# Performance work log

Hardware: AMD Instinct MI355X
Metric: run time of the kernel (lower is better)

## Reference

```python
import jax, jax.numpy as jnp
import numpy as np
import math

B, T, D, La, Lr = 8, 128, 512, 2, 2
H = La + Lr
DK = D // H  # 128
DFF = 4 * D


def _gelu(x):
    # BERT tanh-approx GELU, matching the torch module exactly
    return 0.5 * x * (1.0 + jnp.tanh(math.sqrt(2.0 / math.pi) * (x + 0.044715 * x ** 3)))


def _ln(x, g, b, eps=1e-5):
    mu = jnp.mean(x, axis=-1, keepdims=True)
    var = jnp.mean((x - mu) ** 2, axis=-1, keepdims=True)
    return (x - mu) * jax.lax.rsqrt(var + eps) * g + b


def setup_inputs() -> dict:
    key = jax.random.key(0)
    ks = jax.random.split(key, 16)
    n = lambda k, s, sc=1.0: jax.random.normal(k, s, dtype=jnp.float32) * sc
    return {
        'x': n(ks[0], (B, T, D)),
        'mask': jnp.ones((B, 1, T, T), dtype=jnp.int32),
        'abs_kernel': n(ks[1], (La, B, T, D)),
        'rel_kernel': n(ks[2], (Lr, B, T, T, D)),
        'Wc': n(ks[3], (3, D, D), 0.02), 'bc': jnp.zeros((3, D), jnp.float32),
        'Wpq': n(ks[4], (La, D, DK), 0.02), 'bpq': jnp.zeros((La, DK), jnp.float32),
        'Wpk': n(ks[5], (La, D, DK), 0.02), 'bpk': jnp.zeros((La, DK), jnp.float32),
        'Wrk': n(ks[6], (Lr, D, DK), 0.02), 'brk': jnp.zeros((Lr, DK), jnp.float32),
        'rel_bias': n(ks[7], (Lr, DK), 0.02),
        'Wo': n(ks[8], (D, D), 0.02), 'bo': jnp.zeros((D,), jnp.float32),
        'W1': n(ks[9], (D, DFF), 0.02), 'b1': jnp.zeros((DFF,), jnp.float32),
        'W2': n(ks[10], (DFF, D), 0.02), 'b2': jnp.zeros((D,), jnp.float32),
        'ln1_g': jnp.ones((D,), jnp.float32), 'ln1_b': jnp.zeros((D,), jnp.float32),
        'ln2_g': jnp.ones((D,), jnp.float32), 'ln2_b': jnp.zeros((D,), jnp.float32),
    }


def _attention(h, mask, abs_kernel, rel_kernel, Wc, bc, Wpq, bpq, Wpk, bpk,
               Wrk, brk, rel_bias, Wo, bo):
    b, t = h.shape[0], h.shape[1]
    # content projections: [3,B,T,D] -> [3,B,H,T,DK]
    qkv = jnp.einsum('btd,cde->cbte', h, Wc) + bc[:, None, None, :]
    qkv = qkv.reshape(3, b, t, H, DK).transpose(0, 1, 3, 2, 4)
    q, k, v = qkv[0], qkv[1], qkv[2]
    # absolute-position heads
    Pq = jnp.einsum('abtd,ade->bate', abs_kernel, Wpq) + bpq[None, :, None, :]
    Pk = jnp.einsum('abtd,ade->bate', abs_kernel, Wpk) + bpk[None, :, None, :]
    abs_scores = jnp.einsum('blid,bljd->blij', q[:, :La] + Pq, k[:, :La] + Pk)
    # relative-position heads (R: [B,Lr,T,T,DK])
    R = jnp.einsum('abijd,ade->baije', rel_kernel, Wrk) + brk[None, :, None, None, :]
    Xq = q[:, La:]
    rel_scores = jnp.einsum('blid,bljd->blij', Xq, k[:, La:])
    rel_scores = rel_scores + jnp.einsum('blid,blijd->blij', Xq + rel_bias[None, :, None, :], R)
    scores = jnp.concatenate([abs_scores, rel_scores], axis=1) * (DK ** -0.5)
    scores = jnp.where(mask == 0, jnp.float32(-1e9), scores)
    p_attn = jax.nn.softmax(scores, axis=-1)
    out = jnp.einsum('bhij,bhjd->bhid', p_attn, v)
    out = out.transpose(0, 2, 1, 3).reshape(b, t, H * DK)
    return out @ Wo + bo


def reference(x, mask, abs_kernel, rel_kernel, Wc, bc, Wpq, bpq, Wpk, bpk,
              Wrk, brk, rel_bias, Wo, bo, W1, b1, W2, b2,
              ln1_g, ln1_b, ln2_g, ln2_b):
    # pre-LN sublayer 1: attention
    h = _ln(x, ln1_g, ln1_b)
    x = x + _attention(h, mask, abs_kernel, rel_kernel, Wc, bc, Wpq, bpq,
                       Wpk, bpk, Wrk, brk, rel_bias, Wo, bo)
    # pre-LN sublayer 2: FFN with tanh-GELU
    h2 = _ln(x, ln2_g, ln2_b)
    x = x + (_gelu(h2 @ W1 + b1) @ W2 + b2)
    return x
```

## Files before the change

kernel.cpp:

```cpp
#include <hip/hip_runtime.h>
#include <math.h>

static constexpr int Dc  = 512;
static constexpr int DKc = 128;

typedef __attribute__((ext_vector_type(8))) short short8v;
typedef __attribute__((ext_vector_type(4))) float f32x4;

static __device__ __forceinline__ ushort f2bf(float x) {
  unsigned u = __builtin_bit_cast(unsigned, x);
  unsigned r = (u + 0x7fffu + ((u >> 16) & 1u)) >> 16;
  return (ushort)r;
}

__device__ __forceinline__ float gelu_f(float v) {
  float t = tanhf(0.7978845608028654f * (v + 0.044715f * v * v * v));
  return 0.5f * v * (1.0f + t);
}

__global__ __launch_bounds__(256) void ln_kernel(const float* __restrict__ x,
    const float* __restrict__ g, const float* __restrict__ bb,
    ushort* __restrict__ out)
{
  int gid = blockIdx.x * 256 + threadIdx.x;
  int row = gid >> 6;
  int lane = threadIdx.x & 63;
  const float* xr = x + (size_t)row * Dc + lane * 8;
  float4 a = *(const float4*)xr;
  float4 c = *(const float4*)(xr + 4);
  float s  = a.x + a.y + a.z + a.w + c.x + c.y + c.z + c.w;
  float ss = a.x*a.x + a.y*a.y + a.z*a.z + a.w*a.w
           + c.x*c.x + c.y*c.y + c.z*c.z + c.w*c.w;
  #pragma unroll
  for (int off = 32; off > 0; off >>= 1) {
    s  += __shfl_xor(s, off);
    ss += __shfl_xor(ss, off);
  }
  float mu  = s * (1.0f/512.0f);
  float var = ss * (1.0f/512.0f) - mu*mu;
  float rstd = rsqrtf(var + 1e-5f);
  const float* gp = g + lane*8;
  const float* bp = bb + lane*8;
  float4 g0 = *(const float4*)gp, g1 = *(const float4*)(gp+4);
  float4 b0 = *(const float4*)bp, b1 = *(const float4*)(bp+4);
  union { ushort u[8]; uint4 v; } pk;
  pk.u[0] = f2bf((a.x-mu)*rstd*g0.x + b0.x);
  pk.u[1] = f2bf((a.y-mu)*rstd*g0.y + b0.y);
  pk.u[2] = f2bf((a.z-mu)*rstd*g0.z + b0.z);
  pk.u[3] = f2bf((a.w-mu)*rstd*g0.w + b0.w);
  pk.u[4] = f2bf((c.x-mu)*rstd*g1.x + b1.x);
  pk.u[5] = f2bf((c.y-mu)*rstd*g1.y + b1.y);
  pk.u[6] = f2bf((c.z-mu)*rstd*g1.z + b1.z);
  pk.u[7] = f2bf((c.w-mu)*rstd*g1.w + b1.w);
  *(uint4*)(out + (size_t)row * Dc + lane * 8) = pk.v;
}

struct CvtTasks {
  const float* src[16];
  void* dst[16];
  int rows[16], cols[16], mode[16], aux[16], end[16];
  int n;
};

__global__ __launch_bounds__(256) void cvt_kernel(CvtTasks T)
{
  __shared__ ushort tile[64][65];
  int b = blockIdx.x, t = threadIdx.x;
  int ti = 0;
  while (b >= T.end[ti]) ++ti;
  int lb = b - (ti ? T.end[ti-1] : 0);
  const float* src = T.src[ti];
  int mode = T.mode[ti];
  if (mode == 0) {
    int R = T.rows[ti], C = T.cols[ti];
    int tpr = C >> 6;
    int tyy = lb / tpr, txx = lb - tyy * tpr;
    int r0 = tyy << 6, c0 = txx << 6;
    int lr = t >> 4, lc4 = (t & 15) << 2;
    #pragma unroll
    for (int i = 0; i < 4; ++i) {
      int row = i*16 + lr;
      float4 vv = *(const float4*)(src + (size_t)(r0+row)*C + c0 + lc4);
      tile[row][lc4+0] = f2bf(vv.x);
      tile[row][lc4+1] = f2bf(vv.y);
      tile[row][lc4+2] = f2bf(vv.z);
      tile[row][lc4+3] = f2bf(vv.w);
    }
    __syncthreads();
    ushort* dst = (ushort*)T.dst[ti];
    #pragma unroll
    for (int i = 0; i < 4; ++i) {
      int n = i*16 + lr;
      ushort4 o;
      o.x = tile[lc4+0][n];
      o.y = tile[lc4+1][n];
      o.z = tile[lc4+2][n];
      o.w = tile[lc4+3][n];
      *(ushort4*)(dst + (size_t)(c0+n)*R + r0 + lc4) = o;
    }
  } else if (mode == 1) {
    int idx = lb*2048 + t*8;
    float4 v0 = *(const float4*)(src + idx);
    float4 v1 = *(const float4*)(src + idx + 4);
    union { ushort u[8]; uint4 q; } pk;
    pk.u[0]=f2bf(v0.x); pk.u[1]=f2bf(v0.y); pk.u[2]=f2bf(v0.z); pk.u[3]=f2bf(v0.w);
    pk.u[4]=f2bf(v1.x); pk.u[5]=f2bf(v1.y); pk.u[6]=f2bf(v1.z); pk.u[7]=f2bf(v1.w);
    *(uint4*)((ushort*)T.dst[ti] + idx) = pk.q;
  } else {
    if (t < T.cols[ti]) {
      float* d = (float*)T.dst[ti];
      for (int r = 0; r < T.rows[ti]; ++r)
        d[(size_t)(2*r + T.aux[ti]) * T.cols[ti] + t] = src[(size_t)r * T.cols[ti] + t];
    }
  }
}

template<bool OUT_BF16, bool GELU_>
__device__ __forceinline__ void gemm64_body(
    const ushort* __restrict__ A, int lda,
    const ushort* __restrict__ Bt, int ldb,
    const float* __restrict__ bias,
    void* __restrict__ Cout, int ldc,
    int ksteps, int bm, int bn)
{
  __shared__ __align__(16) char smem[16384];
  char* asB = smem;
  char* bsB = smem + 8192;
  int tid = threadIdx.x;
  int lane = tid & 63, wid = tid >> 6;
  int wr = wid >> 1, wc = wid & 1;
  int l15 = lane & 15, kg = lane >> 4;
  f32x4 acc[2][2] = {};
  const ushort* Ab = A + (size_t)bm * lda;
  const ushort* Bb = Bt + (size_t)bn * ldb;
  int r0 = tid >> 3;
  int c16 = tid & 7;
  int wb0 = r0*128 + ((c16*16) ^ ((r0 & 7) << 4));
  int wb1 = (r0+32)*128 + ((c16*16) ^ ((r0 & 7) << 4));
  for (int ks = 0; ks < ksteps; ++ks) {
    int k0 = ks * 64;
    uint4 ra0 = *(const uint4*)(Ab + (size_t)r0*lda + k0 + c16*8);
    uint4 ra1 = *(const uint4*)(Ab + (size_t)(r0+32)*lda + k0 + c16*8);
    uint4 rb0 = *(const uint4*)(Bb + (size_t)r0*ldb + k0 + c16*8);
    uint4 rb1 = *(const uint4*)(Bb + (size_t)(r0+32)*ldb + k0 + c16*8);
    __syncthreads();
    *(uint4*)(asB + wb0) = ra0;  *(uint4*)(asB + wb1) = ra1;
    *(uint4*)(bsB + wb0) = rb0;  *(uint4*)(bsB + wb1) = rb1;
    __syncthreads();
    #pragma unroll
    for (int half = 0; half < 2; ++half) {
      int cb = half*64 + kg*16;
      short8v av[2], bv[2];
      #pragma unroll
      for (int m = 0; m < 2; ++m) {
        int r = wr*32 + m*16 + l15;
        av[m] = *(const short8v*)(asB + r*128 + (cb ^ ((r & 7) << 4)));
      }
      #pragma unroll
      for (int n = 0; n < 2; ++n) {
        int r = wc*32 + n*16 + l15;
        bv[n] = *(const short8v*)(bsB + r*128 + (cb ^ ((r & 7) << 4)));
      }
      #pragma unroll
      for (int m = 0; m < 2; ++m)
        #pragma unroll
        for (int n = 0; n < 2; ++n)
          acc[m][n] = __builtin_amdgcn_mfma_f32_16x16x32_bf16(av[m], bv[n], acc[m][n], 0, 0, 0);
    }
  }
  int orow0 = bm + wr*32 + kg*4;
  int ocol0 = bn + wc*32 + l15;
  #pragma unroll
  for (int m = 0; m < 2; ++m) {
    #pragma unroll
    for (int r = 0; r < 4; ++r) {
      int row = orow0 + m*16 + r;
      #pragma unroll
      for (int n = 0; n < 2; ++n) {
        int col = ocol0 + n*16;
        float val = acc[m][n][r];
        if (bias) val += bias[col];
        if (GELU_) val = gelu_f(val);
        if (OUT_BF16) ((ushort*)Cout)[(size_t)row*ldc + col] = f2bf(val);
        else          ((float*)Cout)[(size_t)row*ldc + col]  = val;
      }
    }
  }
}

template<bool OUT_BF16, bool GELU_>
__global__ __launch_bounds__(256) void g64(
    const ushort* __restrict__ A, int lda, long Abatch,
    const ushort* __restrict__ Bt, int ldb, long Bbatch,
    const float* __restrict__ bias, int biasStride,
    void* __restrict__ C, int ldc, long Cbatch,
    int ksteps)
{
  int z = blockIdx.z;
  const float* bz = bias ? bias + (size_t)z * biasStride : nullptr;
  void* Cz = OUT_BF16 ? (void*)((ushort*)C + (size_t)z*Cbatch)
                      : (void*)((float*)C + (size_t)z*Cbatch);
  gemm64_body<OUT_BF16, GELU_>(A + (size_t)z*Abatch, lda,
      Bt + (size_t)z*Bbatch, ldb, bz, Cz, ldc, ksteps,
      blockIdx.y*64, blockIdx.x*64);
}

__global__ __launch_bounds__(256) void qkvp_gemm(
    const ushort* __restrict__ h, const ushort* __restrict__ WcT,
    const float* __restrict__ bc, float* __restrict__ qkv,
    const ushort* __restrict__ absb, const ushort* __restrict__ Wp,
    const float* __restrict__ bqk, float* __restrict__ Pqk)
{
  int z = blockIdx.z;
  const ushort *A, *Bt;
  const float* bias;
  float* C;
  int ldc;
  if (z < 3) {
    A = h; Bt = WcT + (size_t)z*262144; bias = bc + z*512;
    C = qkv + (size_t)z*524288; ldc = 512;
  } else {
    if (blockIdx.x >= 2) return;
    int t = z - 3;
    A = absb + (size_t)(t >> 1)*524288;
    Bt = Wp + (size_t)t*65536;
    bias = bqk + t*128;
    C = Pqk + (size_t)t*131072; ldc = 128;
  }
  gemm64_body<false,false>(A, 512, Bt, 512, bias, C, ldc, 8,
      blockIdx.y*64, blockIdx.x*64);
}

__global__ __launch_bounds__(256) void fused_small(
    const float* __restrict__ q, const float* __restrict__ k,
    float* __restrict__ Pqk, const float* __restrict__ rel_bias,
    const float* __restrict__ brk, ushort* __restrict__ uinb,
    float* __restrict__ cvec)
{
  int tid = threadIdx.x;
  if (blockIdx.x < 1024) {
    int idx = blockIdx.x*256 + tid;
    int dk = idx & 127;
    int rest = idx >> 7;
    int m = rest & 1023;
    int a = rest >> 10;
    Pqk[idx + a*131072]     += q[(size_t)m*512 + a*128 + dk];
    Pqk[idx + (a+1)*131072] += k[(size_t)m*512 + a*128 + dk];
  } else {
    int blkk = blockIdx.x - 1024;
    int half = tid >> 7, t = tid & 127;
    int row = blkk*2 + half;
    int l = row >> 10, m = row & 1023;
    float val = q[(size_t)m*512 + (2+l)*128 + t] + rel_bias[l*128 + t];
    uinb[(size_t)row*128 + t] = f2bf(val);
    float p = brk[l*128 + t] * val;
    #pragma unroll
    for (int off = 32; off > 0; off >>= 1) p += __shfl_xor(p, off);
    __shared__ float red[4];
    if ((tid & 63) == 0) red[tid >> 6] = p;
    __syncthreads();
    if (tid == 0)   cvec[row] = red[0] + red[1];
    if (tid == 128) cvec[row] = red[2] + red[3];
  }
}

__global__ __launch_bounds__(256) void relattn_kernel(
    const float* __restrict__ rk, const float* __restrict__ u,
    const float* __restrict__ q, const float* __restrict__ k,
    const float* __restrict__ v, const float* __restrict__ cvec,
    const int* __restrict__ mask, ushort* __restrict__ attnob)
{
  int blk = blockIdx.x;
  int tid = threadIdx.x;
  int i = blk & 127, b = (blk >> 7) & 7, l = blk >> 10, h = 2 + l;
  int m_i = b*128 + i;
  __shared__ float qs[128], sc[128], ps[128], red[64], pvs[2][128], stat[2];
  int wave = tid >> 6, lane = tid & 63;
  const float* ur = u + ((size_t)l*1024 + m_i)*512 + lane*8;
  float4 uu0 = *(const float4*)ur;
  float4 uu1 = *(const float4*)(ur + 4);
  if (tid < 128) qs[tid] = q[(size_t)m_i*512 + h*128 + tid];
  __syncthreads();
  float xq0 = qs[lane*2], xq1 = qs[lane*2+1];
  const float* base = rk + (size_t)blk*65536 + lane*8;
  const float* kb = k + (size_t)(b*128)*512 + h*128 + lane*2;
  #pragma unroll 2
  for (int jj = 0; jj < 32; ++jj) {
    int j = wave*32 + jj;
    const float* r = base + (size_t)j*512;
    float4 r0 = *(const float4*)r;
    float4 r1 = *(const float4*)(r + 4);
    float2 kk = *(const float2*)(kb + (size_t)j*512);
    float s = r0.x*uu0.x + r0.y*uu0.y + r0.z*uu0.z + r0.w*uu0.w
            + r1.x*uu1.x + r1.y*uu1.y + r1.z*uu1.z + r1.w*uu1.w
            + kk.x*xq0 + kk.y*xq1;
    #pragma unroll
    for (int off = 32; off > 0; off >>= 1) s += __shfl_xor(s, off);
    if (lane == 0) sc[j] = s;
  }
  __syncthreads();
  if (tid < 128) {
    float sv = (sc[tid] + cvec[l*1024 + m_i]) * 0.088388347648318447f;
    if (mask[((size_t)(b*128) + i)*128 + tid] == 0) sv = -1e9f;
    sc[tid] = sv;
  }
  __syncthreads();
  if (tid < 64) red[tid] = fmaxf(sc[tid], sc[tid+64]);
  __syncthreads();
  if (tid < 64) {
    float m = red[tid];
    #pragma unroll
    for (int off = 32; off > 0; off >>= 1) m = fmaxf(m, __shfl_xor(m, off));
    if (tid == 0) stat[0] = m;
  }
  __syncthreads();
  if (tid < 128) ps[tid] = __expf(sc[tid] - stat[0]);
  __syncthreads();
  if (tid < 64) red[tid] = ps[tid] + ps[tid+64];
  __syncthreads();
  if (tid < 64) {
    float s = red[tid];
    #pragma unroll
    for (int off = 32; off > 0; off >>= 1) s += __shfl_xor(s, off);
    if (tid == 0) stat[1] = 1.0f / s;
  }
  __syncthreads();
  int hf = tid >> 7, dk = tid & 127;
  const float* vp = v + (size_t)(b*128 + hf*64)*512 + h*128 + dk;
  float o = 0.0f;
  #pragma unroll 4
  for (int jj = 0; jj < 64; ++jj) o += ps[hf*64 + jj] * vp[(size_t)jj*512];
  pvs[hf][dk] = o;
  __syncthreads();
  if (tid < 128)
    attnob[(size_t)m_i*512 + h*128 + tid] = f2bf((pvs[0][tid] + pvs[1][tid]) * stat[1]);
}

__global__ __launch_bounds__(128) void absattn_kernel(
    const float* __restrict__ Pqk, const float* __restrict__ v,
    const int* __restrict__ mask, ushort* __restrict__ attnob)
{
  int blk = blockIdx.x;
  int tid = threadIdx.x;
  int i = blk & 127;
  int bh = blk >> 7;
  int h = bh & 1;
  int b = bh >> 1;
  __shared__ float qsh[128], psh[128], redh[128];
  int m_i = b*128 + i;
  qsh[tid] = Pqk[(size_t)(2*h)*131072 + (size_t)m_i*128 + tid];
  __syncthreads();
  int j = tid, m_j = b*128 + j;
  const float* krow = Pqk + (size_t)(2*h+1)*131072 + (size_t)m_j*128;
  float dot = 0.0f;
  #pragma unroll
  for (int d = 0; d < 128; d += 4) {
    float4 kv = *(const float4*)(krow + d);
    dot += kv.x*qsh[d] + kv.y*qsh[d+1] + kv.z*qsh[d+2] + kv.w*qsh[d+3];
  }
  float s = dot * 0.088388347648318447f;
  if (mask[((size_t)(b*128) + i)*128 + j] == 0) s = -1e9f;
  redh[tid] = s;
  __syncthreads();
  #pragma unroll
  for (int off = 64; off > 0; off >>= 1) {
    if (tid < off) redh[tid] = fmaxf(redh[tid], redh[tid + off]);
    __syncthreads();
  }
  float mx = redh[0];
  __syncthreads();
  float e = __expf(s - mx);
  psh[tid] = e;
  redh[tid] = e;
  __syncthreads();
  #pragma unroll
  for (int off = 64; off > 0; off >>= 1) {
    if (tid < off) redh[tid] += redh[tid + off];
    __syncthreads();
  }
  float inv = 1.0f / redh[0];
  int dk = tid;
  const float* vp = v + (size_t)b*65536 + h*128 + dk;
  float o = 0.0f;
  for (int jj = 0; jj < 128; ++jj) o += psh[jj] * vp[(size_t)jj*512];
  attnob[(size_t)m_i*512 + h*128 + dk] = f2bf(o * inv);
}

__global__ __launch_bounds__(256) void reduce_ln_kernel(
    const float* __restrict__ wpart, const float* __restrict__ bo,
    const float* __restrict__ x, const float* __restrict__ g,
    const float* __restrict__ bb, float* __restrict__ x1,
    ushort* __restrict__ h2)
{
  int gid = blockIdx.x*256 + threadIdx.x;
  int row = gid >> 6, lane = threadIdx.x & 63;
  size_t off = (size_t)row*512 + lane*8;
  float4 a = *(const float4*)(x + off);
  float4 c = *(const float4*)(x + off + 4);
  #pragma unroll
  for (int sk = 0; sk < 4; ++sk) {
    float4 p0 = *(const float4*)(wpart + (size_t)sk*524288 + off);
    float4 p1 = *(const float4*)(wpart + (size_t)sk*524288 + off + 4);
    a.x += p0.x; a.y += p0.y; a.z += p0.z; a.w += p0.w;
    c.x += p1.x; c.y += p1.y; c.z += p1.z; c.w += p1.w;
  }
  float4 bo0 = *(const float4*)(bo + lane*8);
  float4 bo1 = *(const float4*)(bo + lane*8 + 4);
  a.x += bo0.x; a.y += bo0.y; a.z += bo0.z; a.w += bo0.w;
  c.x += bo1.x; c.y += bo1.y; c.z += bo1.z; c.w += bo1.w;
  *(float4*)(x1 + off) = a;
  *(float4*)(x1 + off + 4) = c;
  float s  = a.x + a.y + a.z + a.w + c.x + c.y + c.z + c.w;
  float ss = a.x*a.x + a.y*a.y + a.z*a.z + a.w*a.w
           + c.x*c.x + c.y*c.y + c.z*c.z + c.w*c.w;
  #pragma unroll
  for (int off2 = 32; off2 > 0; off2 >>= 1) {
    s  += __shfl_xor(s, off2);
    ss += __shfl_xor(ss, off2);
  }
  float mu  = s * (1.0f/512.0f);
  float var = ss * (1.0f/512.0f) - mu*mu;
  float rstd = rsqrtf(var + 1e-5f);
  float4 g0 = *(const float4*)(g + lane*8), g1 = *(const float4*)(g + lane*8 + 4);
  float4 b0 = *(const float4*)(bb + lane*8), b1 = *(const float4*)(bb + lane*8 + 4);
  union { ushort u[8]; uint4 v; } pk;
  pk.u[0] = f2bf((a.x-mu)*rstd*g0.x + b0.x);
  pk.u[1] = f2bf((a.y-mu)*rstd*g0.y + b0.y);
  pk.u[2] = f2bf((a.z-mu)*rstd*g0.z + b0.z);
  pk.u[3] = f2bf((a.w-mu)*rstd*g0.w + b0.w);
  pk.u[4] = f2bf((c.x-mu)*rstd*g1.x + b1.x);
  pk.u[5] = f2bf((c.y-mu)*rstd*g1.y + b1.y);
  pk.u[6] = f2bf((c.z-mu)*rstd*g1.z + b1.z);
  pk.u[7] = f2bf((c.w-mu)*rstd*g1.w + b1.w);
  *(uint4*)(h2 + off) = pk.v;
}

__global__ __launch_bounds__(256) void reduce_out_kernel(
    const float* __restrict__ fpart, const float* __restrict__ b2,
    const float* __restrict__ x1, float* __restrict__ out)
{
  int idx = blockIdx.x*256 + threadIdx.x;
  size_t o4 = (size_t)idx*4;
  float4 s = *(const float4*)(x1 + o4);
  #pragma unroll
  for (int sk = 0; sk < 4; ++sk) {
    float4 p = *(const float4*)(fpart + (size_t)sk*524288 + o4);
    s.x += p.x; s.y += p.y; s.z += p.z; s.w += p.w;
  }
  float4 bv = *(const float4*)(b2 + ((idx & 127)*4));
  s.x += bv.x; s.y += bv.y; s.z += bv.z; s.w += bv.w;
  *(float4*)(out + o4) = s;
}

extern "C" void kernel_launch(void* const* d_in, const int* in_sizes, int n_in,
                              void* d_out, int out_size, void* d_ws, size_t ws_size,
                              hipStream_t stream)
{
  const float* x         = (const float*)d_in[0];
  const int*   mask      = (const int*)  d_in[1];
  const float* abs_kernel= (const float*)d_in[2];
  const float* rel_kernel= (const float*)d_in[3];
  const float* Wc        = (const float*)d_in[4];
  const float* bc        = (const float*)d_in[5];
  const float* Wpq       = (const float*)d_in[6];
  const float* bpq       = (const float*)d_in[7];
  const float* Wpk       = (const float*)d_in[8];
  const float* bpk       = (const float*)d_in[9];
  const float* Wrk       = (const float*)d_in[10];
  const float* brk       = (const float*)d_in[11];
  const float* rel_bias  = (const float*)d_in[12];
  const float* Wo        = (const float*)d_in[13];
  const float* bo        = (const float*)d_in[14];
  const float* W1        = (const float*)d_in[15];
  const float* b1        = (const float*)d_in[16];
  const float* W2        = (const float*)d_in[17];
  const float* b2        = (const float*)d_in[18];
  const float* ln1g      = (const float*)d_in[19];
  const float* ln1b      = (const float*)d_in[20];
  const float* ln2g      = (const float*)d_in[21];
  const float* ln2b      = (const float*)d_in[22];

  float* ws = (float*)d_ws;
  float* q      = ws;
  float* kbuf   = ws + 524288;
  float* v      = ws + 1048576;
  float* Pqk    = ws + 1572864;
  float* u      = ws + 2097152;
  float* x1     = ws + 3145728;
  float* cvec   = ws + 3670016;
  float* bqk    = ws + 3672064;
  float* wpart  = ws + 3672576;
  float* fpart  = wpart;
  ushort* bf    = (ushort*)(ws + 5769728);
  ushort* h     = bf;
  ushort* h2    = bf + 524288;
  ushort* uinb  = bf + 1048576;
  ushort* attnob= bf + 1310720;
  ushort* f1    = bf + 1835008;
  ushort* absb  = bf + 3932160;
  ushort* WcT   = bf + 4980736;
  ushort* Wp    = bf + 5767168;
  ushort* Wrkb  = bf + 6029312;
  ushort* WoT   = bf + 6160384;
  ushort* W1T   = bf + 6422528;
  ushort* W2T   = bf + 7471104;
  float* out    = (float*)d_out;

  CvtTasks T{};
  int nb = 0, ti = 0;
  auto addTr = [&](const float* s, ushort* d, int R, int C) {
    T.src[ti]=s; T.dst[ti]=d; T.rows[ti]=R; T.cols[ti]=C; T.mode[ti]=0; T.aux[ti]=0;
    nb += (R/64)*(C/64); T.end[ti]=nb; ++ti;
  };
  auto addCv = [&](const float* s, ushort* d, int n) {
    T.src[ti]=s; T.dst[ti]=d; T.rows[ti]=n; T.cols[ti]=0; T.mode[ti]=1; T.aux[ti]=0;
    nb += n/2048; T.end[ti]=nb; ++ti;
  };
  auto addBi = [&](const float* s, float* d, int aux) {
    T.src[ti]=s; T.dst[ti]=d; T.rows[ti]=2; T.cols[ti]=128; T.mode[ti]=2; T.aux[ti]=aux;
    nb += 1; T.end[ti]=nb; ++ti;
  };
  for (int c = 0; c < 3; ++c) addTr(Wc + (size_t)c*262144, WcT + (size_t)c*262144, 512, 512);
  addTr(Wo, WoT, 512, 512);
  addTr(W1, W1T, 512, 2048);
  addTr(W2, W2T, 2048, 512);
  for (int a = 0; a < 2; ++a) addTr(Wpq + (size_t)a*65536, Wp + (size_t)(2*a)*65536, 512, 128);
  for (int a = 0; a < 2; ++a) addTr(Wpk + (size_t)a*65536, Wp + (size_t)(2*a+1)*65536, 512, 128);
  addCv(abs_kernel, absb, 1048576);
  addCv(Wrk, Wrkb, 131072);
  addBi(bpq, bqk, 0);
  addBi(bpk, bqk, 1);
  T.n = ti;

  cvt_kernel<<<nb, 256, 0, stream>>>(T);

  ln_kernel<<<256, 256, 0, stream>>>(x, ln1g, ln1b, h);

  qkvp_gemm<<<dim3(8,16,7), 256, 0, stream>>>(h, WcT, bc, q, absb, Wp, bqk, Pqk);

  fused_small<<<2048, 256, 0, stream>>>(q, kbuf, Pqk, rel_bias, brk, uinb, cvec);

  g64<false,false><<<dim3(8,16,2), 256, 0, stream>>>(
      uinb, 128, 131072, Wrkb, 128, 65536, nullptr, 0, u, 512, 524288, 2);

  relattn_kernel<<<2048, 256, 0, stream>>>(rel_kernel, u, q, kbuf, v, cvec, mask, attnob);

  absattn_kernel<<<2048, 128, 0, stream>>>(Pqk, v, mask, attnob);

  g64<false,false><<<dim3(8,16,4), 256, 0, stream>>>(
      attnob, 512, 128, WoT, 512, 128, nullptr, 0, wpart, 512, 524288, 2);

  reduce_ln_kernel<<<256, 256, 0, stream>>>(wpart, bo, x, ln2g, ln2b, x1, h2);

  g64<true,true><<<dim3(32,16,1), 256, 0, stream>>>(
      h2, 512, 0, W1T, 512, 0, b1, 0, f1, 2048, 0, 8);

  g64<false,false><<<dim3(8,16,4), 256, 0, stream>>>(
      f1, 2048, 512, W2T, 2048, 512, nullptr, 0, fpart, 512, 524288, 8);

  reduce_out_kernel<<<512, 256, 0, stream>>>(fpart, b2, x1, out);
}
```

Measured before the change: 217.8 us.

## Enlarge GEMM tiles to 128x128 and fuse small kernels to cut launches

Every GEMM tile goes from 64x64 to 128x128, with 4x4 MFMA fragments per wave and 32KB of LDS. LayerNorm-1 becomes a mode of the conversion kernel, the Wrk projection GEMM is folded into the pre-attention kernel, and the relative and absolute attention kernels merge into one launch. The aim is fewer kernel launches and more operand reuse per tile. The cost is far fewer blocks on a 256-CU part (for example 128 blocks for W1), which can leave the GPU underoccupied, plus higher register pressure.

```diff
diff --git a/kernel.cpp b/kernel.cpp
--- a/kernel.cpp
+++ b/kernel.cpp
@@ -1,8 +1,5 @@
 #include <hip/hip_runtime.h>
 #include <math.h>
-
-static constexpr int Dc  = 512;
-static constexpr int DKc = 128;
 
 typedef __attribute__((ext_vector_type(8))) short short8v;
 typedef __attribute__((ext_vector_type(4))) float f32x4;
@@ -18,51 +15,15 @@
   return 0.5f * v * (1.0f + t);
 }
 
-__global__ __launch_bounds__(256) void ln_kernel(const float* __restrict__ x,
-    const float* __restrict__ g, const float* __restrict__ bb,
-    ushort* __restrict__ out)
-{
-  int gid = blockIdx.x * 256 + threadIdx.x;
-  int row = gid >> 6;
-  int lane = threadIdx.x & 63;
-  const float* xr = x + (size_t)row * Dc + lane * 8;
-  float4 a = *(const float4*)xr;
-  float4 c = *(const float4*)(xr + 4);
-  float s  = a.x + a.y + a.z + a.w + c.x + c.y + c.z + c.w;
-  float ss = a.x*a.x + a.y*a.y + a.z*a.z + a.w*a.w
-           + c.x*c.x + c.y*c.y + c.z*c.z + c.w*c.w;
-  #pragma unroll
-  for (int off = 32; off > 0; off >>= 1) {
-    s  += __shfl_xor(s, off);
-    ss += __shfl_xor(ss, off);
-  }
-  float mu  = s * (1.0f/512.0f);
-  float var = ss * (1.0f/512.0f) - mu*mu;
-  float rstd = rsqrtf(var + 1e-5f);
-  const float* gp = g + lane*8;
-  const float* bp = bb + lane*8;
-  float4 g0 = *(const float4*)gp, g1 = *(const float4*)(gp+4);
-  float4 b0 = *(const float4*)bp, b1 = *(const float4*)(bp+4);
-  union { ushort u[8]; uint4 v; } pk;
-  pk.u[0] = f2bf((a.x-mu)*rstd*g0.x + b0.x);
-  pk.u[1] = f2bf((a.y-mu)*rstd*g0.y + b0.y);
-  pk.u[2] = f2bf((a.z-mu)*rstd*g0.z + b0.z);
-  pk.u[3] = f2bf((a.w-mu)*rstd*g0.w + b0.w);
-  pk.u[4] = f2bf((c.x-mu)*rstd*g1.x + b1.x);
-  pk.u[5] = f2bf((c.y-mu)*rstd*g1.y + b1.y);
-  pk.u[6] = f2bf((c.z-mu)*rstd*g1.z + b1.z);
-  pk.u[7] = f2bf((c.w-mu)*rstd*g1.w + b1.w);
-  *(uint4*)(out + (size_t)row * Dc + lane * 8) = pk.v;
-}
-
 struct CvtTasks {
   const float* src[16];
   void* dst[16];
   int rows[16], cols[16], mode[16], aux[16], end[16];
-  int n;
 };
 
-__global__ __launch_bounds__(256) void cvt_kernel(CvtTasks T)
+__global__ __launch_bounds__(256) void cvt_kernel(CvtTasks T,
+    const float* __restrict__ lnx, const float* __restrict__ lng,
+    const float* __restrict__ lnb, ushort* __restrict__ lnout)
 {
   __shared__ ushort tile[64][65];
   int b = blockIdx.x, t = threadIdx.x;
@@ -106,77 +67,113 @@
     pk.u[0]=f2bf(v0.x); pk.u[1]=f2bf(v0.y); pk.u[2]=f2bf(v0.z); pk.u[3]=f2bf(v0.w);
     pk.u[4]=f2bf(v1.x); pk.u[5]=f2bf(v1.y); pk.u[6]=f2bf(v1.z); pk.u[7]=f2bf(v1.w);
     *(uint4*)((ushort*)T.dst[ti] + idx) = pk.q;
-  } else {
+  } else if (mode == 2) {
     if (t < T.cols[ti]) {
       float* d = (float*)T.dst[ti];
       for (int r = 0; r < T.rows[ti]; ++r)
         d[(size_t)(2*r + T.aux[ti]) * T.cols[ti] + t] = src[(size_t)r * T.cols[ti] + t];
     }
+  } else {
+    int row = lb*4 + (t >> 6);
+    int lane = t & 63;
+    const float* xr = lnx + (size_t)row*512 + lane*8;
+    float4 a = *(const float4*)xr;
+    float4 c = *(const float4*)(xr + 4);
+    float s  = a.x + a.y + a.z + a.w + c.x + c.y + c.z + c.w;
+    float ss = a.x*a.x + a.y*a.y + a.z*a.z + a.w*a.w
+             + c.x*c.x + c.y*c.y + c.z*c.z + c.w*c.w;
+    #pragma unroll
+    for (int off = 32; off > 0; off >>= 1) {
+      s  += __shfl_xor(s, off);
+      ss += __shfl_xor(ss, off);
+    }
+    float mu  = s * (1.0f/512.0f);
+    float var = ss * (1.0f/512.0f) - mu*mu;
+    float rstd = rsqrtf(var + 1e-5f);
+    float4 g0 = *(const float4*)(lng + lane*8), g1 = *(const float4*)(lng + lane*8 + 4);
+    float4 b0 = *(const float4*)(lnb + lane*8), b1 = *(const float4*)(lnb + lane*8 + 4);
+    union { ushort u[8]; uint4 v; } pk;
+    pk.u[0] = f2bf((a.x-mu)*rstd*g0.x + b0.x);
+    pk.u[1] = f2bf((a.y-mu)*rstd*g0.y + b0.y);
+    pk.u[2] = f2bf((a.z-mu)*rstd*g0.z + b0.z);
+    pk.u[3] = f2bf((a.w-mu)*rstd*g0.w + b0.w);
+    pk.u[4] = f2bf((c.x-mu)*rstd*g1.x + b1.x);
+    pk.u[5] = f2bf((c.y-mu)*rstd*g1.y + b1.y);
+    pk.u[6] = f2bf((c.z-mu)*rstd*g1.z + b1.z);
+    pk.u[7] = f2bf((c.w-mu)*rstd*g1.w + b1.w);
+    *(uint4*)(lnout + (size_t)row*512 + lane*8) = pk.v;
   }
 }
 
 template<bool OUT_BF16, bool GELU_>
-__device__ __forceinline__ void gemm64_body(
+__device__ __forceinline__ void gemm128_body(
     const ushort* __restrict__ A, int lda,
     const ushort* __restrict__ Bt, int ldb,
     const float* __restrict__ bias,
     void* __restrict__ Cout, int ldc,
     int ksteps, int bm, int bn)
 {
-  __shared__ __align__(16) char smem[16384];
+  __shared__ __align__(16) char smem[32768];
   char* asB = smem;
-  char* bsB = smem + 8192;
+  char* bsB = smem + 16384;
   int tid = threadIdx.x;
   int lane = tid & 63, wid = tid >> 6;
   int wr = wid >> 1, wc = wid & 1;
   int l15 = lane & 15, kg = lane >> 4;
-  f32x4 acc[2][2] = {};
+  int frA = wr*64 + l15;
+  int frB = wc*64 + l15;
+  f32x4 acc[4][4] = {};
   const ushort* Ab = A + (size_t)bm * lda;
   const ushort* Bb = Bt + (size_t)bn * ldb;
-  int r0 = tid >> 3;
-  int c16 = tid & 7;
-  int wb0 = r0*128 + ((c16*16) ^ ((r0 & 7) << 4));
-  int wb1 = (r0+32)*128 + ((c16*16) ^ ((r0 & 7) << 4));
+  int srow[4], spc[4];
+  #pragma unroll
+  for (int i = 0; i < 4; ++i) { int g = i*256 + tid; srow[i] = g >> 3; spc[i] = g & 7; }
   for (int ks = 0; ks < ksteps; ++ks) {
     int k0 = ks * 64;
-    uint4 ra0 = *(const uint4*)(Ab + (size_t)r0*lda + k0 + c16*8);
-    uint4 ra1 = *(const uint4*)(Ab + (size_t)(r0+32)*lda + k0 + c16*8);
-    uint4 rb0 = *(const uint4*)(Bb + (size_t)r0*ldb + k0 + c16*8);
-    uint4 rb1 = *(const uint4*)(Bb + (size_t)(r0+32)*ldb + k0 + c16*8);
-    __syncthreads();
-    *(uint4*)(asB + wb0) = ra0;  *(uint4*)(asB + wb1) = ra1;
-    *(uint4*)(bsB + wb0) = rb0;  *(uint4*)(bsB + wb1) = rb1;
-    __syncthreads();
-    #pragma unroll
-    for (int half = 0; half < 2; ++half) {
-      int cb = half*64 + kg*16;
-      short8v av[2], bv[2];
-      #pragma unroll
-      for (int m = 0; m < 2; ++m) {
-        int r = wr*32 + m*16 + l15;
-        av[m] = *(const short8v*)(asB + r*128 + (cb ^ ((r & 7) << 4)));
+    uint4 ra[4], rb[4];
+    #pragma unroll
+    for (int i = 0; i < 4; ++i) {
+      ra[i] = *(const uint4*)(Ab + (size_t)srow[i]*lda + k0 + spc[i]*8);
+      rb[i] = *(const uint4*)(Bb + (size_t)srow[i]*ldb + k0 + spc[i]*8);
+    }
+    __syncthreads();
+    #pragma unroll
+    for (int i = 0; i < 4; ++i) {
+      int wbyte = srow[i]*128 + ((spc[i]*16) ^ ((srow[i]&7)<<4));
+      *(uint4*)(asB + wbyte) = ra[i];
+      *(uint4*)(bsB + wbyte) = rb[i];
+    }
+    __syncthreads();
+    #pragma unroll
+    for (int ks2 = 0; ks2 < 2; ++ks2) {
+      short8v av[4], bv[4];
+      int cb = ks2*64 + kg*16;
+      #pragma unroll
+      for (int m = 0; m < 4; ++m) {
+        int r = frA + m*16;
+        av[m] = *(const short8v*)(asB + r*128 + (cb ^ ((r&7)<<4)));
       }
       #pragma unroll
-      for (int n = 0; n < 2; ++n) {
-        int r = wc*32 + n*16 + l15;
-        bv[n] = *(const short8v*)(bsB + r*128 + (cb ^ ((r & 7) << 4)));
+      for (int n = 0; n < 4; ++n) {
+        int r = frB + n*16;
+        bv[n] = *(const short8v*)(bsB + r*128 + (cb ^ ((r&7)<<4)));
       }
       #pragma unroll
-      for (int m = 0; m < 2; ++m)
+      for (int m = 0; m < 4; ++m)
         #pragma unroll
-        for (int n = 0; n < 2; ++n)
+        for (int n = 0; n < 4; ++n)
           acc[m][n] = __builtin_amdgcn_mfma_f32_16x16x32_bf16(av[m], bv[n], acc[m][n], 0, 0, 0);
     }
   }
-  int orow0 = bm + wr*32 + kg*4;
-  int ocol0 = bn + wc*32 + l15;
+  int orow0 = bm + wr*64 + kg*4;
+  int ocol0 = bn + wc*64 + l15;
   #pragma unroll
-  for (int m = 0; m < 2; ++m) {
+  for (int m = 0; m < 4; ++m) {
     #pragma unroll
     for (int r = 0; r < 4; ++r) {
       int row = orow0 + m*16 + r;
       #pragma unroll
-      for (int n = 0; n < 2; ++n) {
+      for (int n = 0; n < 4; ++n) {
         int col = ocol0 + n*16;
         float val = acc[m][n][r];
         if (bias) val += bias[col];
@@ -189,7 +186,7 @@
 }
 
 template<bool OUT_BF16, bool GELU_>
-__global__ __launch_bounds__(256) void g64(
+__global__ __launch_bounds__(256) void g128(
     const ushort* __restrict__ A, int lda, long Abatch,
     const ushort* __restrict__ Bt, int ldb, long Bbatch,
     const float* __restrict__ bias, int biasStride,
@@ -200,9 +197,9 @@
   const float* bz = bias ? bias + (size_t)z * biasStride : nullptr;
   void* Cz = OUT_BF16 ? (void*)((ushort*)C + (size_t)z*Cbatch)
                       : (void*)((float*)C + (size_t)z*Cbatch);
-  gemm64_body<OUT_BF16, GELU_>(A + (size_t)z*Abatch, lda,
+  gemm128_body<OUT_BF16, GELU_>(A + (size_t)z*Abatch, lda,
       Bt + (size_t)z*Bbatch, ldb, bz, Cz, ldc, ksteps,
-      blockIdx.y*64, blockIdx.x*64);
+      blockIdx.y*128, blockIdx.x*128);
 }
 
 __global__ __launch_bounds__(256) void qkvp_gemm(
@@ -212,178 +209,241 @@
     const float* __restrict__ bqk, float* __restrict__ Pqk)
 {
   int z = blockIdx.z;
-  const ushort *A, *Bt;
-  const float* bias;
-  float* C;
-  int ldc;
   if (z < 3) {
-    A = h; Bt = WcT + (size_t)z*262144; bias = bc + z*512;
-    C = qkv + (size_t)z*524288; ldc = 512;
+    gemm128_body<false,false>(h, 512, WcT + (size_t)z*262144, 512, bc + z*512,
+        qkv + (size_t)z*524288, 512, 8, blockIdx.y*128, blockIdx.x*128);
   } else {
-    if (blockIdx.x >= 2) return;
+    if (blockIdx.x != 0) return;
     int t = z - 3;
-    A = absb + (size_t)(t >> 1)*524288;
-    Bt = Wp + (size_t)t*65536;
-    bias = bqk + t*128;
-    C = Pqk + (size_t)t*131072; ldc = 128;
-  }
-  gemm64_body<false,false>(A, 512, Bt, 512, bias, C, ldc, 8,
-      blockIdx.y*64, blockIdx.x*64);
-}
-
-__global__ __launch_bounds__(256) void fused_small(
-    const float* __restrict__ q, const float* __restrict__ k,
-    float* __restrict__ Pqk, const float* __restrict__ rel_bias,
-    const float* __restrict__ brk, ushort* __restrict__ uinb,
+    gemm128_body<false,false>(absb + (size_t)(t>>1)*524288, 512,
+        Wp + (size_t)t*65536, 512, bqk + t*128,
+        Pqk + (size_t)t*131072, 128, 8, blockIdx.y*128, 0);
+  }
+}
+
+__global__ __launch_bounds__(256) void fused_pre(
+    const float* __restrict__ q, float* __restrict__ Pqk,
+    const float* __restrict__ rel_bias, const float* __restrict__ brk,
+    const ushort* __restrict__ Wrkb, float* __restrict__ u,
     float* __restrict__ cvec)
 {
+  int blk = blockIdx.x;
   int tid = threadIdx.x;
-  if (blockIdx.x < 1024) {
-    int idx = blockIdx.x*256 + tid;
+  if (blk < 64) {
+    int l = blk >> 5;
+    int rem = blk & 31;
+    int bm = ((rem >> 2) & 7) * 128;
+    int bn = (rem & 3) * 128;
+    __shared__ __align__(16) char smem[32768];
+    char* asB = smem;
+    char* bsB = smem + 16384;
+    int lane = tid & 63, wid = tid >> 6;
+    int wr = wid >> 1, wc = wid & 1;
+    int l15 = lane & 15, kg = lane >> 4;
+    int frA = wr*64 + l15, frB = wc*64 + l15;
+    f32x4 acc[4][4] = {};
+    const ushort* Bb = Wrkb + (size_t)l*65536 + (size_t)bn*128;
+    int srow[4], spc[4];
+    #pragma unroll
+    for (int i = 0; i < 4; ++i) { int g = i*256 + tid; srow[i] = g >> 3; spc[i] = g & 7; }
+    for (int ks = 0; ks < 2; ++ks) {
+      int k0 = ks * 64;
+      uint4 ra[4], rb[4];
+      #pragma unroll
+      for (int i = 0; i < 4; ++i) {
+        int m = bm + srow[i];
+        int e0 = k0 + spc[i]*8;
+        const float* qp = q + (size_t)m*512 + (2+l)*128 + e0;
+        float4 qa = *(const float4*)qp;
+        float4 qb = *(const float4*)(qp + 4);
+        const float* rp = rel_bias + l*128 + e0;
+        float4 r0 = *(const float4*)rp;
+        float4 r1 = *(const float4*)(rp + 4);
+        union { ushort s[8]; uint4 v; } pk;
+        pk.s[0]=f2bf(qa.x+r0.x); pk.s[1]=f2bf(qa.y+r0.y);
+        pk.s[2]=f2bf(qa.z+r0.z); pk.s[3]=f2bf(qa.w+r0.w);
+        pk.s[4]=f2bf(qb.x+r1.x); pk.s[5]=f2bf(qb.y+r1.y);
+        pk.s[6]=f2bf(qb.z+r1.z); pk.s[7]=f2bf(qb.w+r1.w);
+        ra[i] = pk.v;
+        rb[i] = *(const uint4*)(Bb + (size_t)srow[i]*128 + k0 + spc[i]*8);
+      }
+      __syncthreads();
+      #pragma unroll
+      for (int i = 0; i < 4; ++i) {
+        int wbyte = srow[i]*128 + ((spc[i]*16) ^ ((srow[i]&7)<<4));
+        *(uint4*)(asB + wbyte) = ra[i];
+        *(uint4*)(bsB + wbyte) = rb[i];
+      }
+      __syncthreads();
+      #pragma unroll
+      for (int ks2 = 0; ks2 < 2; ++ks2) {
+        short8v av[4], bv[4];
+        int cb = ks2*64 + kg*16;
+        #pragma unroll
+        for (int m = 0; m < 4; ++m) {
+          int r = frA + m*16;
+          av[m] = *(const short8v*)(asB + r*128 + (cb ^ ((r&7)<<4)));
+        }
+        #pragma unroll
+        for (int n = 0; n < 4; ++n) {
+          int r = frB + n*16;
+          bv[n] = *(const short8v*)(bsB + r*128 + (cb ^ ((r&7)<<4)));
+        }
+        #pragma unroll
+        for (int m = 0; m < 4; ++m)
+          #pragma unroll
+          for (int n = 0; n < 4; ++n)
+            acc[m][n] = __builtin_amdgcn_mfma_f32_16x16x32_bf16(av[m], bv[n], acc[m][n], 0, 0, 0);
+      }
+    }
+    float* Cz = u + (size_t)l*524288;
+    int orow0 = bm + wr*64 + kg*4;
+    int ocol0 = bn + wc*64 + l15;
+    #pragma unroll
+    for (int m = 0; m < 4; ++m)
+      #pragma unroll
+      for (int r = 0; r < 4; ++r) {
+        int row = orow0 + m*16 + r;
+        #pragma unroll
+        for (int n = 0; n < 4; ++n)
+          Cz[(size_t)row*512 + ocol0 + n*16] = acc[m][n][r];
+      }
+  } else if (blk < 1088) {
+    int idx = (blk - 64)*256 + tid;
     int dk = idx & 127;
     int rest = idx >> 7;
     int m = rest & 1023;
     int a = rest >> 10;
     Pqk[idx + a*131072]     += q[(size_t)m*512 + a*128 + dk];
-    Pqk[idx + (a+1)*131072] += k[(size_t)m*512 + a*128 + dk];
+    Pqk[idx + (a+1)*131072] += q[(size_t)(1024 + m)*512 + a*128 + dk];
   } else {
-    int blkk = blockIdx.x - 1024;
-    int half = tid >> 7, t = tid & 127;
-    int row = blkk*2 + half;
+    int row = (blk - 1088)*2 + (tid >> 7);
     int l = row >> 10, m = row & 1023;
+    int t = tid & 127, hf = tid >> 7;
     float val = q[(size_t)m*512 + (2+l)*128 + t] + rel_bias[l*128 + t];
-    uinb[(size_t)row*128 + t] = f2bf(val);
     float p = brk[l*128 + t] * val;
     #pragma unroll
     for (int off = 32; off > 0; off >>= 1) p += __shfl_xor(p, off);
-    __shared__ float red[4];
-    if ((tid & 63) == 0) red[tid >> 6] = p;
-    __syncthreads();
-    if (tid == 0)   cvec[row] = red[0] + red[1];
-    if (tid == 128) cvec[row] = red[2] + red[3];
-  }
-}
-
-__global__ __launch_bounds__(256) void relattn_kernel(
+    __shared__ float red[2][2];
+    if ((tid & 63) == 0) red[hf][(tid >> 6) & 1] = p;
+    __syncthreads();
+    if (t == 0) cvec[row] = red[hf][0] + red[hf][1];
+  }
+}
+
+__global__ __launch_bounds__(256) void attn_kernel(
     const float* __restrict__ rk, const float* __restrict__ u,
     const float* __restrict__ q, const float* __restrict__ k,
     const float* __restrict__ v, const float* __restrict__ cvec,
-    const int* __restrict__ mask, ushort* __restrict__ attnob)
+    const float* __restrict__ Pqk, const int* __restrict__ mask,
+    ushort* __restrict__ attnob)
 {
   int blk = blockIdx.x;
   int tid = threadIdx.x;
-  int i = blk & 127, b = (blk >> 7) & 7, l = blk >> 10, h = 2 + l;
-  int m_i = b*128 + i;
-  __shared__ float qs[128], sc[128], ps[128], red[64], pvs[2][128], stat[2];
-  int wave = tid >> 6, lane = tid & 63;
-  const float* ur = u + ((size_t)l*1024 + m_i)*512 + lane*8;
-  float4 uu0 = *(const float4*)ur;
-  float4 uu1 = *(const float4*)(ur + 4);
-  if (tid < 128) qs[tid] = q[(size_t)m_i*512 + h*128 + tid];
-  __syncthreads();
-  float xq0 = qs[lane*2], xq1 = qs[lane*2+1];
-  const float* base = rk + (size_t)blk*65536 + lane*8;
-  const float* kb = k + (size_t)(b*128)*512 + h*128 + lane*2;
-  #pragma unroll 2
-  for (int jj = 0; jj < 32; ++jj) {
-    int j = wave*32 + jj;
-    const float* r = base + (size_t)j*512;
-    float4 r0 = *(const float4*)r;
-    float4 r1 = *(const float4*)(r + 4);
-    float2 kk = *(const float2*)(kb + (size_t)j*512);
-    float s = r0.x*uu0.x + r0.y*uu0.y + r0.z*uu0.z + r0.w*uu0.w
-            + r1.x*uu1.x + r1.y*uu1.y + r1.z*uu1.z + r1.w*uu1.w
-            + kk.x*xq0 + kk.y*xq1;
-    #pragma unroll
-    for (int off = 32; off > 0; off >>= 1) s += __shfl_xor(s, off);
-    if (lane == 0) sc[j] = s;
-  }
-  __syncthreads();
-  if (tid < 128) {
-    float sv = (sc[tid] + cvec[l*1024 + m_i]) * 0.088388347648318447f;
-    if (mask[((size_t)(b*128) + i)*128 + tid] == 0) sv = -1e9f;
-    sc[tid] = sv;
-  }
-  __syncthreads();
-  if (tid < 64) red[tid] = fmaxf(sc[tid], sc[tid+64]);
-  __syncthreads();
-  if (tid < 64) {
-    float m = red[tid];
-    #pragma unroll
-    for (int off = 32; off > 0; off >>= 1) m = fmaxf(m, __shfl_xor(m, off));
-    if (tid == 0) stat[0] = m;
-  }
-  __syncthreads();
-  if (tid < 128) ps[tid] = __expf(sc[tid] - stat[0]);
-  __syncthreads();
-  if (tid < 64) red[tid] = ps[tid] + ps[tid+64];
-  __syncthreads();
-  if (tid < 64) {
-    float s = red[tid];
-    #pragma unroll
-    for (int off = 32; off > 0; off >>= 1) s += __shfl_xor(s, off);
-    if (tid == 0) stat[1] = 1.0f / s;
-  }
-  __syncthreads();
-  int hf = tid >> 7, dk = tid & 127;
-  const float* vp = v + (size_t)(b*128 + hf*64)*512 + h*128 + dk;
-  float o = 0.0f;
-  #pragma unroll 4
-  for (int jj = 0; jj < 64; ++jj) o += ps[hf*64 + jj] * vp[(size_t)jj*512];
-  pvs[hf][dk] = o;
-  __syncthreads();
-  if (tid < 128)
-    attnob[(size_t)m_i*512 + h*128 + tid] = f2bf((pvs[0][tid] + pvs[1][tid]) * stat[1]);
-}
-
-__global__ __launch_bounds__(128) void absattn_kernel(
-    const float* __restrict__ Pqk, const float* __restrict__ v,
-    const int* __restrict__ mask, ushort* __restrict__ attnob)
-{
-  int blk = blockIdx.x;
-  int tid = threadIdx.x;
-  int i = blk & 127;
-  int bh = blk >> 7;
-  int h = bh & 1;
-  int b = bh >> 1;
-  __shared__ float qsh[128], psh[128], redh[128];
-  int m_i = b*128 + i;
-  qsh[tid] = Pqk[(size_t)(2*h)*131072 + (size_t)m_i*128 + tid];
-  __syncthreads();
-  int j = tid, m_j = b*128 + j;
-  const float* krow = Pqk + (size_t)(2*h+1)*131072 + (size_t)m_j*128;
-  float dot = 0.0f;
-  #pragma unroll
-  for (int d = 0; d < 128; d += 4) {
-    float4 kv = *(const float4*)(krow + d);
-    dot += kv.x*qsh[d] + kv.y*qsh[d+1] + kv.z*qsh[d+2] + kv.w*qsh[d+3];
-  }
-  float s = dot * 0.088388347648318447f;
-  if (mask[((size_t)(b*128) + i)*128 + j] == 0) s = -1e9f;
-  redh[tid] = s;
-  __syncthreads();
-  #pragma unroll
-  for (int off = 64; off > 0; off >>= 1) {
-    if (tid < off) redh[tid] = fmaxf(redh[tid], redh[tid + off]);
-    __syncthreads();
-  }
-  float mx = redh[0];
-  __syncthreads();
-  float e = __expf(s - mx);
-  psh[tid] = e;
-  redh[tid] = e;
-  __syncthreads();
-  #pragma unroll
-  for (int off = 64; off > 0; off >>= 1) {
-    if (tid < off) redh[tid] += redh[tid + off];
-    __syncthreads();
-  }
-  float inv = 1.0f / redh[0];
-  int dk = tid;
-  const float* vp = v + (size_t)b*65536 + h*128 + dk;
-  float o = 0.0f;
-  for (int jj = 0; jj < 128; ++jj) o += psh[jj] * vp[(size_t)jj*512];
-  attnob[(size_t)m_i*512 + h*128 + dk] = f2bf(o * inv);
+  if (blk < 2048) {
+    int i = blk & 127, b = (blk >> 7) & 7, l = blk >> 10, h = 2 + l;
+    int m_i = b*128 + i;
+    __shared__ float qs[128], sc[128], ps[128], red[64], pvs[2][128], stat[2];
+    int wave = tid >> 6, lane = tid & 63;
+    const float* ur = u + ((size_t)l*1024 + m_i)*512 + lane*8;
+    float4 uu0 = *(const float4*)ur;
+    float4 uu1 = *(const float4*)(ur + 4);
+    if (tid < 128) qs[tid] = q[(size_t)m_i*512 + h*128 + tid];
+    __syncthreads();
+    float xq0 = qs[lane*2], xq1 = qs[lane*2+1];
+    const float* base = rk + (size_t)blk*65536 + lane*8;
+    const float* kb = k + (size_t)(b*128)*512 + h*128 + lane*2;
+    #pragma unroll 4
+    for (int jj = 0; jj < 32; ++jj) {
+      int j = wave*32 + jj;
+      const float* r = base + (size_t)j*512;
+      float4 r0 = *(const float4*)r;
+      float4 r1 = *(const float4*)(r + 4);
+      float2 kk = *(const float2*)(kb + (size_t)j*512);
+      float s = r0.x*uu0.x + r0.y*uu0.y + r0.z*uu0.z + r0.w*uu0.w
+              + r1.x*uu1.x + r1.y*uu1.y + r1.z*uu1.z + r1.w*uu1.w
+              + kk.x*xq0 + kk.y*xq1;
+      #pragma unroll
+      for (int off = 32; off > 0; off >>= 1) s += __shfl_xor(s, off);
+      if (lane == 0) sc[j] = s;
+    }
+    __syncthreads();
+    if (tid < 128) {
+      float sv = (sc[tid] + cvec[l*1024 + m_i]) * 0.088388347648318447f;
+      if (mask[((size_t)(b*128) + i)*128 + tid] == 0) sv = -1e9f;
+      sc[tid] = sv;
+    }
+    __syncthreads();
+    if (tid < 64) red[tid] = fmaxf(sc[tid], sc[tid+64]);
+    __syncthreads();
+    if (tid < 64) {
+      float m = red[tid];
+      #pragma unroll
+      for (int off = 32; off > 0; off >>= 1) m = fmaxf(m, __shfl_xor(m, off));
+      if (tid == 0) stat[0] = m;
+    }
+    __syncthreads();
+    if (tid < 128) ps[tid] = __expf(sc[tid] - stat[0]);
+    __syncthreads();
+    if (tid < 64) red[tid] = ps[tid] + ps[tid+64];
+    __syncthreads();
+    if (tid < 64) {
+      float s = red[tid];
+      #pragma unroll
+      for (int off = 32; off > 0; off >>= 1) s += __shfl_xor(s, off);
+      if (tid == 0) stat[1] = 1.0f / s;
+    }
+    __syncthreads();
+    int hf = tid >> 7, dk = tid & 127;
+    const float* vp = v + (size_t)(b*128 + hf*64)*512 + h*128 + dk;
+    float o = 0.0f;
+    #pragma unroll 4
+    for (int jj = 0; jj < 64; ++jj) o += ps[hf*64 + jj] * vp[(size_t)jj*512];
+    pvs[hf][dk] = o;
+    __syncthreads();
+    if (tid < 128)
+      attnob[(size_t)m_i*512 + h*128 + tid] = f2bf((pvs[0][tid] + pvs[1][tid]) * stat[1]);
+  } else {
+    int ab = blk - 2048;
+    int hf = tid >> 7, t = tid & 127;
+    int i  = (ab & 63)*2 + hf;
+    int bh = ab >> 6;
+    int h  = bh & 1, b = bh >> 1;
+    __shared__ float qsh[2][128], psh[2][128], redm[2][2], reds[2][2];
+    int m_i = b*128 + i;
+    qsh[hf][t] = Pqk[(size_t)(2*h)*131072 + (size_t)m_i*128 + t];
+    __syncthreads();
+    int m_j = b*128 + t;
+    const float* krow = Pqk + (size_t)(2*h+1)*131072 + (size_t)m_j*128;
+    float dot = 0.0f;
+    #pragma unroll
+    for (int d = 0; d < 128; d += 4) {
+      float4 kv = *(const float4*)(krow + d);
+      dot += kv.x*qsh[hf][d] + kv.y*qsh[hf][d+1] + kv.z*qsh[hf][d+2] + kv.w*qsh[hf][d+3];
+    }
+    float s = dot * 0.088388347648318447f;
+    if (mask[((size_t)(b*128) + i)*128 + t] == 0) s = -1e9f;
+    float mx = s;
+    #pragma unroll
+    for (int off = 32; off > 0; off >>= 1) mx = fmaxf(mx, __shfl_xor(mx, off));
+    int w2 = (tid >> 6) & 1;
+    if ((tid & 63) == 0) redm[hf][w2] = mx;
+    __syncthreads();
+    mx = fmaxf(redm[hf][0], redm[hf][1]);
+    float e = __expf(s - mx);
+    psh[hf][t] = e;
+    float sum = e;
+    #pragma unroll
+    for (int off = 32; off > 0; off >>= 1) sum += __shfl_xor(sum, off);
+    if ((tid & 63) == 0) reds[hf][w2] = sum;
+    __syncthreads();
+    float inv = 1.0f / (reds[hf][0] + reds[hf][1]);
+    const float* vp = v + (size_t)b*65536 + h*128 + t;
+    float o = 0.0f;
+    #pragma unroll 4
+    for (int jj = 0; jj < 128; ++jj) o += psh[hf][jj] * vp[(size_t)jj*512];
+    attnob[(size_t)m_i*512 + h*128 + t] = f2bf(o * inv);
+  }
 }
 
 __global__ __launch_bounds__(256) void reduce_ln_kernel(
@@ -494,16 +554,15 @@
   ushort* bf    = (ushort*)(ws + 5769728);
   ushort* h     = bf;
   ushort* h2    = bf + 524288;
-  ushort* uinb  = bf + 1048576;
-  ushort* attnob= bf + 1310720;
-  ushort* f1    = bf + 1835008;
-  ushort* absb  = bf + 3932160;
-  ushort* WcT   = bf + 4980736;
-  ushort* Wp    = bf + 5767168;
-  ushort* Wrkb  = bf + 6029312;
-  ushort* WoT   = bf + 6160384;
-  ushort* W1T   = bf + 6422528;
-  ushort* W2T   = bf + 7471104;
+  ushort* attnob= bf + 1048576;
+  ushort* f1    = bf + 1572864;
+  ushort* absb  = bf + 3670016;
+  ushort* WcT   = bf + 4718592;
+  ushort* Wp    = bf + 5505024;
+  ushort* Wrkb  = bf + 5767168;
+  ushort* WoT   = bf + 5898240;
+  ushort* W1T   = bf + 6160384;
+  ushort* W2T   = bf + 7208960;
   float* out    = (float*)d_out;
 
   CvtTasks T{};
@@ -530,32 +589,25 @@
   addCv(Wrk, Wrkb, 131072);
   addBi(bpq, bqk, 0);
   addBi(bpk, bqk, 1);
-  T.n = ti;
-
-  cvt_kernel<<<nb, 256, 0, stream>>>(T);
-
-  ln_kernel<<<256, 256, 0, stream>>>(x, ln1g, ln1b, h);
-
-  qkvp_gemm<<<dim3(8,16,7), 256, 0, stream>>>(h, WcT, bc, q, absb, Wp, bqk, Pqk);
-
-  fused_small<<<2048, 256, 0, stream>>>(q, kbuf, Pqk, rel_bias, brk, uinb, cvec);
-
-  g64<false,false><<<dim3(8,16,2), 256, 0, stream>>>(
-      uinb, 128, 131072, Wrkb, 128, 65536, nullptr, 0, u, 512, 524288, 2);
-
-  relattn_kernel<<<2048, 256, 0, stream>>>(rel_kernel, u, q, kbuf, v, cvec, mask, attnob);
-
-  absattn_kernel<<<2048, 128, 0, stream>>>(Pqk, v, mask, attnob);
-
-  g64<false,false><<<dim3(8,16,4), 256, 0, stream>>>(
+  T.src[ti]=x; T.dst[ti]=h; T.mode[ti]=3; nb += 256; T.end[ti]=nb; ++ti;
+
+  cvt_kernel<<<nb, 256, 0, stream>>>(T, x, ln1g, ln1b, h);
+
+  qkvp_gemm<<<dim3(4,8,7), 256, 0, stream>>>(h, WcT, bc, q, absb, Wp, bqk, Pqk);
+
+  fused_pre<<<2112, 256, 0, stream>>>(q, Pqk, rel_bias, brk, Wrkb, u, cvec);
+
+  attn_kernel<<<3072, 256, 0, stream>>>(rel_kernel, u, q, kbuf, v, cvec, Pqk, mask, attnob);
+
+  g128<false,false><<<dim3(4,8,4), 256, 0, stream>>>(
       attnob, 512, 128, WoT, 512, 128, nullptr, 0, wpart, 512, 524288, 2);
 
   reduce_ln_kernel<<<256, 256, 0, stream>>>(wpart, bo, x, ln2g, ln2b, x1, h2);
 
-  g64<true,true><<<dim3(32,16,1), 256, 0, stream>>>(
+  g128<true,true><<<dim3(16,8,1), 256, 0, stream>>>(
       h2, 512, 0, W1T, 512, 0, b1, 0, f1, 2048, 0, 8);
 
-  g64<false,false><<<dim3(8,16,4), 256, 0, stream>>>(
+  g128<false,false><<<dim3(4,8,4), 256, 0, stream>>>(
       f1, 2048, 512, W2T, 2048, 512, nullptr, 0, fpart, 512, 524288, 8);
 
   reduce_out_kernel<<<512, 256, 0, stream>>>(fpart, b2, x1, out);
```

Measured after the change: 280.2 us. 28.6% more time.
